# Performance work log

Hardware: AMD Instinct MI355X
Metric: run time of the kernel (lower is better)

Reference implementation:

```python
import jax, jax.numpy as jnp
import numpy as np

EMBED_DIM = 1024
NUM_HEAD = 16
HEAD_DIM = EMBED_DIM // NUM_HEAD


def setup_inputs() -> dict:
    key = jax.random.key(0)
    ks = jax.random.split(key, 9)
    B, S, D = 2, 2048, EMBED_DIM
    scale = 1.0 / np.sqrt(D)
    x = jax.random.normal(ks[0], (B, S, D), dtype=jnp.float32)
    Wq = jax.random.normal(ks[1], (D, D), dtype=jnp.float32) * scale
    bq = jnp.zeros((D,), jnp.float32)
    Wk = jax.random.normal(ks[2], (D, D), dtype=jnp.float32) * scale
    bk = jnp.zeros((D,), jnp.float32)
    Wv = jax.random.normal(ks[3], (D, D), dtype=jnp.float32) * scale
    bv = jnp.zeros((D,), jnp.float32)
    Wfc = jax.random.normal(ks[4], (D, D), dtype=jnp.float32) * scale
    bfc = jnp.zeros((D,), jnp.float32)
    return {"x": x, "Wq": Wq, "bq": bq, "Wk": Wk, "bk": bk,
            "Wv": Wv, "bv": bv, "Wfc": Wfc, "bfc": bfc}


def _split_heads(t):
    B, S, D = t.shape
    return t.reshape(B, S, NUM_HEAD, HEAD_DIM).transpose(0, 2, 1, 3)  # b nh s hd


def reference(x, Wq, bq, Wk, bk, Wv, bv, Wfc, bfc):
    # torch nn.Linear: y = x @ W.T + b
    q = _split_heads(x @ Wq.T + bq)   # [b, nh, s, hd]
    k = _split_heads(x @ Wk.T + bk)   # [b, nh, s, hd]
    v = _split_heads(x @ Wv.T + bv)   # [b, nh, s, hd]
    # Gram matrix K^T K per (batch, head): [b, nh, hd, hd]
    gram = jnp.einsum('bnsh,bnsk->bnhk', k, k)
    gram_inv = jnp.linalg.inv(gram)
    # score = Q (K^T K)^{-1} K^T : [b, nh, s, s]
    q_proj = jnp.einsum('bnsh,bnhk->bnsk', q, gram_inv)
    score = jnp.einsum('bnsk,bntk->bnst', q_proj, k)
    attn = jax.nn.softmax(score / jnp.sqrt(jnp.float32(EMBED_DIM)), axis=-1)
    out = jnp.einsum('bnst,bnth->bnsh', attn, v)  # [b, nh, s, hd]
    B, _, S, _ = out.shape
    out = out.transpose(0, 2, 1, 3).reshape(B, S, EMBED_DIM)
    return out @ Wfc.T + bfc
```

## Files before the change

### kernel.cpp

```cpp
#include <hip/hip_runtime.h>
#include <cstddef>
#include <cstdint>

#define S_LEN 2048
#define NHEAD 16
#define HDIM  64
#define EMB   1024
#define MROWS 4096

typedef short bf16x8 __attribute__((ext_vector_type(8)));
typedef float f32x4 __attribute__((ext_vector_type(4)));

__device__ __forceinline__ unsigned short f2bf(float f) {
  union { float f; unsigned u; } v; v.f = f;
  return (unsigned short)((v.u + 0x8000u) >> 16);
}
__device__ __forceinline__ unsigned pack2bf(float a, float b) {
  union { float f; unsigned u; } x, y; x.f = a; y.f = b;
  return ((x.u + 0x8000u) >> 16) | ((y.u + 0x8000u) & 0xFFFF0000u);
}

__device__ __forceinline__ f32x4 fzero() {
  f32x4 z = {0.0f, 0.0f, 0.0f, 0.0f};
  return z;
}

__global__ __launch_bounds__(256) void cast_kernel(
    const float* __restrict__ x, const float* __restrict__ Wq,
    const float* __restrict__ Wk, const float* __restrict__ Wv,
    const float* __restrict__ Wfc, unsigned short* __restrict__ dst)
{
  size_t idx8 = (size_t)(blockIdx.x * 256 + threadIdx.x) * 8;
  unsigned seg = (unsigned)(idx8 >> 20);
  const float* src;
  size_t off;
  if (seg < 4) { src = x; off = idx8; }
  else {
    const float* w4[4] = {Wq, Wk, Wv, Wfc};
    src = w4[seg - 4];
    off = idx8 & 0xFFFFFu;
  }
  float4 a = *(const float4*)&src[off];
  float4 b = *(const float4*)&src[off + 4];
  uint4 p;
  p.x = pack2bf(a.x, a.y);
  p.y = pack2bf(a.z, a.w);
  p.z = pack2bf(b.x, b.y);
  p.w = pack2bf(b.z, b.w);
  *(uint4*)&dst[idx8] = p;
}

__global__ __launch_bounds__(256) void gemm_qkv(
    const unsigned short* __restrict__ A, const unsigned short* __restrict__ Wall,
    const float* __restrict__ bq, const float* __restrict__ bk,
    const float* __restrict__ bv, unsigned short* __restrict__ Qhd,
    unsigned short* __restrict__ Khd, unsigned short* __restrict__ KTd,
    unsigned short* __restrict__ VTd)
{
  __shared__ short As[128][40];
  __shared__ short Bs[128][40];
  const int z = blockIdx.z;
  const unsigned short* B = Wall + (size_t)z * 1048576;
  const float* bias = (z == 0) ? bq : (z == 1) ? bk : bv;
  unsigned short* Yh = (z == 0) ? Qhd : (z == 1) ? Khd : nullptr;
  unsigned short* Yt = (z == 1) ? KTd : (z == 2) ? VTd : nullptr;
  const int K = EMB;
  const int t = threadIdx.x;
  const int lane = t & 63, w = t >> 6;
  const int quad = lane >> 4, l16 = lane & 15;
  const int wr = w >> 1, wc = w & 1;
  const int m0 = blockIdx.y * 128, n0 = blockIdx.x * 128;
  const int sr = t >> 2, sk = (t & 3) * 8;

  f32x4 acc[4][4];
#pragma unroll
  for (int i = 0; i < 4; ++i)
#pragma unroll
    for (int j = 0; j < 4; ++j) acc[i][j] = fzero();

  float4 pa0 = *(const float4*)&A[(size_t)(m0 + sr) * K + sk];
  float4 pa1 = *(const float4*)&A[(size_t)(m0 + 64 + sr) * K + sk];
  float4 pb0 = *(const float4*)&B[(size_t)(n0 + sr) * K + sk];
  float4 pb1 = *(const float4*)&B[(size_t)(n0 + 64 + sr) * K + sk];

  for (int k0 = 0; k0 < K; k0 += 32) {
    __syncthreads();
    *(float4*)&As[sr][sk] = pa0;
    *(float4*)&As[64 + sr][sk] = pa1;
    *(float4*)&Bs[sr][sk] = pb0;
    *(float4*)&Bs[64 + sr][sk] = pb1;
    __syncthreads();
    if (k0 + 32 < K) {
      pa0 = *(const float4*)&A[(size_t)(m0 + sr) * K + k0 + 32 + sk];
      pa1 = *(const float4*)&A[(size_t)(m0 + 64 + sr) * K + k0 + 32 + sk];
      pb0 = *(const float4*)&B[(size_t)(n0 + sr) * K + k0 + 32 + sk];
      pb1 = *(const float4*)&B[(size_t)(n0 + 64 + sr) * K + k0 + 32 + sk];
    }
    bf16x8 af[4], bfr[4];
#pragma unroll
    for (int i = 0; i < 4; ++i)
      af[i] = *(const bf16x8*)&As[64 * wr + 16 * i + l16][quad * 8];
#pragma unroll
    for (int j = 0; j < 4; ++j)
      bfr[j] = *(const bf16x8*)&Bs[64 * wc + 16 * j + l16][quad * 8];
#pragma unroll
    for (int i = 0; i < 4; ++i)
#pragma unroll
      for (int j = 0; j < 4; ++j)
        acc[i][j] = __builtin_amdgcn_mfma_f32_16x16x32_bf16(af[i], bfr[j], acc[i][j], 0, 0, 0);
  }

#pragma unroll
  for (int i = 0; i < 4; ++i) {
    int mb = m0 + 64 * wr + 16 * i + quad * 4;
#pragma unroll
    for (int j = 0; j < 4; ++j) {
      int n = n0 + 64 * wc + 16 * j + l16;
      float bvv = bias[n];
      int h = n >> 6, d = n & 63;
      if (Yh) {
#pragma unroll
        for (int r = 0; r < 4; ++r) {
          int m = mb + r;
          int b = m >> 11, s = m & 2047;
          Yh[((size_t)(b * NHEAD + h)) * 131072 + (size_t)s * 64 + d] =
              f2bf(acc[i][j][r] + bvv);
        }
      }
      if (Yt) {
        int b = mb >> 11, s = mb & 2047;
        uint2 pk;
        pk.x = pack2bf(acc[i][j][0] + bvv, acc[i][j][1] + bvv);
        pk.y = pack2bf(acc[i][j][2] + bvv, acc[i][j][3] + bvv);
        *(uint2*)&Yt[((size_t)(b * NHEAD + h)) * 131072 + (size_t)d * S_LEN + s] = pk;
      }
    }
  }
}

__global__ __launch_bounds__(256) void gemm_fc(
    const unsigned short* __restrict__ A, const unsigned short* __restrict__ B,
    const float* __restrict__ bias, float* __restrict__ Yf)
{
  __shared__ short As[128][40];
  __shared__ short Bs[128][40];
  const int K = EMB, N = EMB;
  const int t = threadIdx.x;
  const int lane = t & 63, w = t >> 6;
  const int quad = lane >> 4, l16 = lane & 15;
  const int wr = w >> 1, wc = w & 1;
  const int m0 = blockIdx.y * 128, n0 = blockIdx.x * 128;
  const int sr = t >> 2, sk = (t & 3) * 8;

  f32x4 acc[4][4];
#pragma unroll
  for (int i = 0; i < 4; ++i)
#pragma unroll
    for (int j = 0; j < 4; ++j) acc[i][j] = fzero();

  float4 pa0 = *(const float4*)&A[(size_t)(m0 + sr) * K + sk];
  float4 pa1 = *(const float4*)&A[(size_t)(m0 + 64 + sr) * K + sk];
  float4 pb0 = *(const float4*)&B[(size_t)(n0 + sr) * K + sk];
  float4 pb1 = *(const float4*)&B[(size_t)(n0 + 64 + sr) * K + sk];

  for (int k0 = 0; k0 < K; k0 += 32) {
    __syncthreads();
    *(float4*)&As[sr][sk] = pa0;
    *(float4*)&As[64 + sr][sk] = pa1;
    *(float4*)&Bs[sr][sk] = pb0;
    *(float4*)&Bs[64 + sr][sk] = pb1;
    __syncthreads();
    if (k0 + 32 < K) {
      pa0 = *(const float4*)&A[(size_t)(m0 + sr) * K + k0 + 32 + sk];
      pa1 = *(const float4*)&A[(size_t)(m0 + 64 + sr) * K + k0 + 32 + sk];
      pb0 = *(const float4*)&B[(size_t)(n0 + sr) * K + k0 + 32 + sk];
      pb1 = *(const float4*)&B[(size_t)(n0 + 64 + sr) * K + k0 + 32 + sk];
    }
    bf16x8 af[4], bfr[4];
#pragma unroll
    for (int i = 0; i < 4; ++i)
      af[i] = *(const bf16x8*)&As[64 * wr + 16 * i + l16][quad * 8];
#pragma unroll
    for (int j = 0; j < 4; ++j)
      bfr[j] = *(const bf16x8*)&Bs[64 * wc + 16 * j + l16][quad * 8];
#pragma unroll
    for (int i = 0; i < 4; ++i)
#pragma unroll
      for (int j = 0; j < 4; ++j)
        acc[i][j] = __builtin_amdgcn_mfma_f32_16x16x32_bf16(af[i], bfr[j], acc[i][j], 0, 0, 0);
  }

#pragma unroll
  for (int i = 0; i < 4; ++i) {
    int mb = m0 + 64 * wr + 16 * i + quad * 4;
#pragma unroll
    for (int j = 0; j < 4; ++j) {
      int n = n0 + 64 * wc + 16 * j + l16;
      float bvv = bias[n];
#pragma unroll
      for (int r = 0; r < 4; ++r)
        Yf[(size_t)(mb + r) * N + n] = acc[i][j][r] + bvv;
    }
  }
}

__global__ __launch_bounds__(256) void gram_mfma(
    const unsigned short* __restrict__ KTh, float* __restrict__ gram_p)
{
  __shared__ short KTs[64][136];
  const int t = threadIdx.x;
  const int lane = t & 63, w = t >> 6;
  const int quad = lane >> 4, l16 = lane & 15;
  const int bh = blockIdx.x >> 2, part = blockIdx.x & 3;
  const unsigned short* Kb = KTh + (size_t)bh * 131072 + part * 512;

  f32x4 gacc[4];
#pragma unroll
  for (int j = 0; j < 4; ++j) gacc[j] = fzero();

  const int rv = t >> 4, cv = (t & 15) * 8;
  for (int st = 0; st < 4; ++st) {
    float4 vv[4];
#pragma unroll
    for (int r = 0; r < 4; ++r)
      vv[r] = *(const float4*)&Kb[(size_t)(rv + 16 * r) * S_LEN + st * 128 + cv];
    __syncthreads();
#pragma unroll
    for (int r = 0; r < 4; ++r)
      *(float4*)&KTs[rv + 16 * r][cv] = vv[r];
    __syncthreads();
#pragma unroll
    for (int c = 0; c < 4; ++c) {
      bf16x8 ai = *(const bf16x8*)&KTs[16 * w + l16][32 * c + quad * 8];
#pragma unroll
      for (int jb = 0; jb < 4; ++jb) {
        bf16x8 bj = *(const bf16x8*)&KTs[16 * jb + l16][32 * c + quad * 8];
        gacc[jb] = __builtin_amdgcn_mfma_f32_16x16x32_bf16(ai, bj, gacc[jb], 0, 0, 0);
      }
    }
  }
#pragma unroll
  for (int jb = 0; jb < 4; ++jb)
#pragma unroll
    for (int r = 0; r < 4; ++r)
      gram_p[(size_t)blockIdx.x * 4096 +
             (size_t)(16 * w + quad * 4 + r) * 64 + 16 * jb + l16] = gacc[jb][r];
}

__global__ __launch_bounds__(256) void inv_kernel(
    const float* __restrict__ gram_p, unsigned short* __restrict__ ginv)
{
  __shared__ float As[64][68];
  __shared__ float prow[2][64];
  __shared__ float fcol[2][64];
  const int bh = blockIdx.x;
  const int t = threadIdx.x;
  const int r = t >> 2;
  const int c0 = (t & 3) * 16;
  const float* G = gram_p + (size_t)bh * 4 * 4096;

  float4 g[4];
#pragma unroll
  for (int jj = 0; jj < 4; ++jj) {
    int off = r * 64 + c0 + 4 * jj;
    float4 s0 = *(const float4*)&G[off];
    float4 s1 = *(const float4*)&G[4096 + off];
    float4 s2 = *(const float4*)&G[8192 + off];
    float4 s3 = *(const float4*)&G[12288 + off];
    g[jj].x = (s0.x + s1.x) + (s2.x + s3.x);
    g[jj].y = (s0.y + s1.y) + (s2.y + s3.y);
    g[jj].z = (s0.z + s1.z) + (s2.z + s3.z);
    g[jj].w = (s0.w + s1.w) + (s2.w + s3.w);
    *(float4*)&As[r][c0 + 4 * jj] = g[jj];
  }
  if (c0 == 0) fcol[0][r] = g[0].x;
  if (r == 0) {
#pragma unroll
    for (int jj = 0; jj < 4; ++jj) *(float4*)&prow[0][c0 + 4 * jj] = g[jj];
  }
  __syncthreads();

  for (int k = 0; k < 64; ++k) {
    const int kb = k & 1;
    const float f = fcol[kb][r];
    const float ip = 1.0f / fcol[kb][k];
    const float fi = f * ip;
    const bool pr = (r == k);
    float4 nv[4];
#pragma unroll
    for (int jj = 0; jj < 4; ++jj) {
      float4 a = *(const float4*)&As[r][c0 + 4 * jj];
      float4 p = *(const float4*)&prow[kb][c0 + 4 * jj];
      float4 o;
      if (pr) {
        o.x = p.x * ip; o.y = p.y * ip; o.z = p.z * ip; o.w = p.w * ip;
      } else {
        o.x = fmaf(-fi, p.x, a.x); o.y = fmaf(-fi, p.y, a.y);
        o.z = fmaf(-fi, p.z, a.z); o.w = fmaf(-fi, p.w, a.w);
      }
      const int cb = c0 + 4 * jj;
      const float kv = pr ? ip : -fi;
      if (cb == k) o.x = kv;
      if (cb + 1 == k) o.y = kv;
      if (cb + 2 == k) o.z = kv;
      if (cb + 3 == k) o.w = kv;
      *(float4*)&As[r][c0 + 4 * jj] = o;
      nv[jj] = o;
    }
    if (k < 63) {
      const int nk = k + 1, nb = nk & 1;
      if (nk >= c0 && nk < c0 + 16) fcol[nb][r] = As[r][nk];
      if (r == nk) {
#pragma unroll
        for (int jj = 0; jj < 4; ++jj) *(float4*)&prow[nb][c0 + 4 * jj] = nv[jj];
      }
    }
    __syncthreads();
  }

  unsigned short* O = ginv + (size_t)bh * 4096;
#pragma unroll
  for (int jj = 0; jj < 4; ++jj) {
    float4 v = *(const float4*)&As[r][c0 + 4 * jj];
    uint2 pk;
    pk.x = pack2bf(v.x, v.y);
    pk.y = pack2bf(v.z, v.w);
    *(uint2*)&O[r * 64 + c0 + 4 * jj] = pk;
  }
}

__global__ __launch_bounds__(256) void flash_mfma(
    const unsigned short* __restrict__ Qh, const unsigned short* __restrict__ Kh,
    const unsigned short* __restrict__ VTh, const unsigned short* __restrict__ Ginv,
    unsigned short* __restrict__ AO)
{
  __shared__ short Qps[64 * 72];
  __shared__ short Ps[2][64 * 72];
  __shared__ float Lred[4][64];
  const int t = threadIdx.x;
  const int lane = t & 63, w = t >> 6;
  const int quad = lane >> 4, l16 = lane & 15;
  const int qt = blockIdx.x, bh = blockIdx.y;
  const unsigned short* Qb = Qh + (size_t)bh * 131072;
  const unsigned short* Kb = Kh + (size_t)bh * 131072;
  const unsigned short* Vb = VTh + (size_t)bh * 131072;
  const unsigned short* Gb = Ginv + (size_t)bh * 4096;

  {
    bf16x8 aq[2];
#pragma unroll
    for (int c = 0; c < 2; ++c)
      aq[c] = *(const bf16x8*)&Qb[(size_t)(qt * 64 + 16 * w + l16) * 64 + 32 * c + 8 * quad];
    f32x4 qacc[4];
#pragma unroll
    for (int nb = 0; nb < 4; ++nb) qacc[nb] = fzero();
#pragma unroll
    for (int c = 0; c < 2; ++c) {
#pragma unroll
      for (int nb = 0; nb < 4; ++nb) {
        bf16x8 bg = *(const bf16x8*)&Gb[(size_t)(16 * nb + l16) * 64 + 32 * c + 8 * quad];
        qacc[nb] = __builtin_amdgcn_mfma_f32_16x16x32_bf16(aq[c], bg, qacc[nb], 0, 0, 0);
      }
    }
#pragma unroll
    for (int nb = 0; nb < 4; ++nb)
#pragma unroll
      for (int r = 0; r < 4; ++r)
        Qps[(16 * w + 4 * quad + r) * 72 + 16 * nb + l16] =
            (short)f2bf(qacc[nb][r] * 0.03125f);
  }
  __syncthreads();

  f32x4 oacc[4];
#pragma unroll
  for (int qb = 0; qb < 4; ++qb) oacc[qb] = fzero();
  float lsum[4] = {0.0f, 0.0f, 0.0f, 0.0f};

  for (int kt = 0; kt < 32; ++kt) {
    bf16x8 ak[2];
#pragma unroll
    for (int c = 0; c < 2; ++c)
      ak[c] = *(const bf16x8*)&Kb[(size_t)(kt * 64 + 16 * w + l16) * 64 + 32 * c + 8 * quad];
    f32x4 sacc[4];
#pragma unroll
    for (int qb = 0; qb < 4; ++qb) sacc[qb] = fzero();
#pragma unroll
    for (int c = 0; c < 2; ++c) {
#pragma unroll
      for (int qb = 0; qb < 4; ++qb) {
        bf16x8 bq = *(const bf16x8*)&Qps[(16 * qb + l16) * 72 + 32 * c + 8 * quad];
        sacc[qb] = __builtin_amdgcn_mfma_f32_16x16x32_bf16(ak[c], bq, sacc[qb], 0, 0, 0);
      }
    }
    short* Pbuf = &Ps[kt & 1][0];
#pragma unroll
    for (int qb = 0; qb < 4; ++qb) {
      float e0 = __expf(sacc[qb][0]);
      float e1 = __expf(sacc[qb][1]);
      float e2 = __expf(sacc[qb][2]);
      float e3 = __expf(sacc[qb][3]);
      lsum[qb] += (e0 + e1) + (e2 + e3);
      uint2 pk;
      pk.x = pack2bf(e0, e1);
      pk.y = pack2bf(e2, e3);
      *(uint2*)&Pbuf[(16 * qb + l16) * 72 + 16 * w + 4 * quad] = pk;
    }
    __syncthreads();

    bf16x8 av[2];
#pragma unroll
    for (int c = 0; c < 2; ++c)
      av[c] = *(const bf16x8*)&Vb[(size_t)(16 * w + l16) * S_LEN + kt * 64 + 32 * c + 8 * quad];
#pragma unroll
    for (int c = 0; c < 2; ++c) {
#pragma unroll
      for (int qb = 0; qb < 4; ++qb) {
        bf16x8 bp = *(const bf16x8*)&Pbuf[(16 * qb + l16) * 72 + 32 * c + 8 * quad];
        oacc[qb] = __builtin_amdgcn_mfma_f32_16x16x32_bf16(av[c], bp, oacc[qb], 0, 0, 0);
      }
    }
  }

#pragma unroll
  for (int qb = 0; qb < 4; ++qb) {
    lsum[qb] += __shfl_xor(lsum[qb], 16, 64);
    lsum[qb] += __shfl_xor(lsum[qb], 32, 64);
  }
  if (lane < 16)
#pragma unroll
    for (int qb = 0; qb < 4; ++qb) Lred[w][qb * 16 + l16] = lsum[qb];
  __syncthreads();
  if (t < 64)
    Lred[0][t] = 1.0f / (Lred[0][t] + Lred[1][t] + Lred[2][t] + Lred[3][t]);
  __syncthreads();

  const int b = bh >> 4, h = bh & 15;
#pragma unroll
  for (int qb = 0; qb < 4; ++qb) {
    float li = Lred[0][16 * qb + l16];
    int s = qt * 64 + 16 * qb + l16;
    size_t base = (size_t)b * S_LEN * EMB + (size_t)s * EMB + h * 64 + 16 * w + 4 * quad;
#pragma unroll
    for (int r = 0; r < 4; ++r)
      AO[base + r] = f2bf(oacc[qb][r] * li);
  }
}

extern "C" void kernel_launch(void* const* d_in, const int* in_sizes, int n_in,
                              void* d_out, int out_size, void* d_ws, size_t ws_size,
                              hipStream_t stream) {
  (void)in_sizes; (void)n_in; (void)out_size; (void)ws_size;
  const float* x   = (const float*)d_in[0];
  const float* Wq  = (const float*)d_in[1];
  const float* bq  = (const float*)d_in[2];
  const float* Wk  = (const float*)d_in[3];
  const float* bk  = (const float*)d_in[4];
  const float* Wv  = (const float*)d_in[5];
  const float* bv  = (const float*)d_in[6];
  const float* Wfc = (const float*)d_in[7];
  const float* bfc = (const float*)d_in[8];
  float* out = (float*)d_out;

  unsigned short* xb   = (unsigned short*)d_ws;
  unsigned short* Wqb  = xb + (size_t)4194304;
  unsigned short* Wfcb = Wqb + 3 * 1048576;
  unsigned short* Qhd  = Wfcb + 1048576;
  unsigned short* Khd  = Qhd + 4194304;
  unsigned short* KTd  = Khd + 4194304;
  unsigned short* VTd  = KTd + 4194304;
  unsigned short* AOd  = VTd + 4194304;
  float* gram_p        = (float*)(AOd + 4194304);
  unsigned short* ginv = (unsigned short*)(gram_p + 524288);

  cast_kernel<<<4096, 256, 0, stream>>>(x, Wq, Wk, Wv, Wfc, xb);
  gemm_qkv<<<dim3(8, 32, 3), 256, 0, stream>>>(xb, Wqb, bq, bk, bv,
                                               Qhd, Khd, KTd, VTd);
  gram_mfma<<<128, 256, 0, stream>>>(KTd, gram_p);
  inv_kernel<<<32, 256, 0, stream>>>(gram_p, ginv);
  flash_mfma<<<dim3(S_LEN / 64, 32), 256, 0, stream>>>(Qhd, Khd, VTd, ginv, AOd);
  gemm_fc<<<dim3(8, 32), 256, 0, stream>>>(AOd, Wfcb, bfc, out);
}
```

Measured before the change: 285.9 us.

## Drop K transpose buffer, stage V transpose via LDS, tune flash and fc kernels

Removes the separate transposed-K output from the QKV GEMM, so the gram kernel reads row-major K and transposes it in shared memory. V^T is now written through an LDS staging tile with 16-byte coalesced stores. The flash kernel keeps Q fragments in registers, prefetches the next K tile, swaps exp for exp2 with a log2e-folded scale, remaps blocks for L2 locality, sets an occupancy hint and stages its output through LDS for vectorized stores. The fc GEMM uses a 64-wide N tile to double the block count. These changes target global memory traffic, uncoalesced writes and load latency, at the cost of more shared memory and some LDS bank conflicts in the gram transpose.

Result: faster. 280.1 us (-2.0%).

```diff
diff --git a/kernel.cpp b/kernel.cpp
--- a/kernel.cpp
+++ b/kernel.cpp
@@ -54,16 +54,14 @@
     const unsigned short* __restrict__ A, const unsigned short* __restrict__ Wall,
     const float* __restrict__ bq, const float* __restrict__ bk,
     const float* __restrict__ bv, unsigned short* __restrict__ Qhd,
-    unsigned short* __restrict__ Khd, unsigned short* __restrict__ KTd,
-    unsigned short* __restrict__ VTd)
+    unsigned short* __restrict__ Khd, unsigned short* __restrict__ VTd)
 {
   __shared__ short As[128][40];
   __shared__ short Bs[128][40];
+  __shared__ short Ts[64][136];
   const int z = blockIdx.z;
   const unsigned short* B = Wall + (size_t)z * 1048576;
   const float* bias = (z == 0) ? bq : (z == 1) ? bk : bv;
-  unsigned short* Yh = (z == 0) ? Qhd : (z == 1) ? Khd : nullptr;
-  unsigned short* Yt = (z == 1) ? KTd : (z == 2) ? VTd : nullptr;
   const int K = EMB;
   const int t = threadIdx.x;
   const int lane = t & 63, w = t >> 6;
@@ -110,15 +108,16 @@
         acc[i][j] = __builtin_amdgcn_mfma_f32_16x16x32_bf16(af[i], bfr[j], acc[i][j], 0, 0, 0);
   }
 
-#pragma unroll
-  for (int i = 0; i < 4; ++i) {
-    int mb = m0 + 64 * wr + 16 * i + quad * 4;
-#pragma unroll
-    for (int j = 0; j < 4; ++j) {
-      int n = n0 + 64 * wc + 16 * j + l16;
-      float bvv = bias[n];
-      int h = n >> 6, d = n & 63;
-      if (Yh) {
+  if (z < 2) {
+    unsigned short* Yh = (z == 0) ? Qhd : Khd;
+#pragma unroll
+    for (int i = 0; i < 4; ++i) {
+      int mb = m0 + 64 * wr + 16 * i + quad * 4;
+#pragma unroll
+      for (int j = 0; j < 4; ++j) {
+        int n = n0 + 64 * wc + 16 * j + l16;
+        float bvv = bias[n];
+        int h = n >> 6, d = n & 63;
 #pragma unroll
         for (int r = 0; r < 4; ++r) {
           int m = mb + r;
@@ -127,13 +126,35 @@
               f2bf(acc[i][j][r] + bvv);
         }
       }
-      if (Yt) {
-        int b = mb >> 11, s = mb & 2047;
-        uint2 pk;
-        pk.x = pack2bf(acc[i][j][0] + bvv, acc[i][j][1] + bvv);
-        pk.y = pack2bf(acc[i][j][2] + bvv, acc[i][j][3] + bvv);
-        *(uint2*)&Yt[((size_t)(b * NHEAD + h)) * 131072 + (size_t)d * S_LEN + s] = pk;
-      }
+    }
+  } else {
+#pragma unroll
+    for (int hh = 0; hh < 2; ++hh) {
+      __syncthreads();
+      if (wc == hh) {
+#pragma unroll
+        for (int i = 0; i < 4; ++i)
+#pragma unroll
+          for (int j = 0; j < 4; ++j) {
+            int n = n0 + 64 * wc + 16 * j + l16;
+            float bvv = bias[n];
+            int dl = 16 * j + l16;
+            uint2 pk;
+            pk.x = pack2bf(acc[i][j][0] + bvv, acc[i][j][1] + bvv);
+            pk.y = pack2bf(acc[i][j][2] + bvv, acc[i][j][3] + bvv);
+            *(uint2*)&Ts[dl][64 * wr + 16 * i + 4 * quad] = pk;
+          }
+      }
+      __syncthreads();
+      int dl = t >> 2, s0 = (t & 3) * 32;
+      int n = n0 + 64 * hh + dl;
+      int h = n >> 6, d = n & 63;
+      int b = m0 >> 11, sbase = (m0 & 2047) + s0;
+      unsigned short* dst =
+          &VTd[((size_t)(b * NHEAD + h)) * 131072 + (size_t)d * S_LEN + sbase];
+#pragma unroll
+      for (int k2 = 0; k2 < 4; ++k2)
+        *(uint4*)&dst[8 * k2] = *(const uint4*)&Ts[dl][s0 + 8 * k2];
     }
   }
 }
@@ -143,50 +164,47 @@
     const float* __restrict__ bias, float* __restrict__ Yf)
 {
   __shared__ short As[128][40];
-  __shared__ short Bs[128][40];
+  __shared__ short Bs[64][40];
   const int K = EMB, N = EMB;
   const int t = threadIdx.x;
   const int lane = t & 63, w = t >> 6;
   const int quad = lane >> 4, l16 = lane & 15;
   const int wr = w >> 1, wc = w & 1;
-  const int m0 = blockIdx.y * 128, n0 = blockIdx.x * 128;
+  const int m0 = blockIdx.y * 128, n0 = blockIdx.x * 64;
   const int sr = t >> 2, sk = (t & 3) * 8;
 
-  f32x4 acc[4][4];
+  f32x4 acc[4][2];
 #pragma unroll
   for (int i = 0; i < 4; ++i)
 #pragma unroll
-    for (int j = 0; j < 4; ++j) acc[i][j] = fzero();
+    for (int j = 0; j < 2; ++j) acc[i][j] = fzero();
 
   float4 pa0 = *(const float4*)&A[(size_t)(m0 + sr) * K + sk];
   float4 pa1 = *(const float4*)&A[(size_t)(m0 + 64 + sr) * K + sk];
   float4 pb0 = *(const float4*)&B[(size_t)(n0 + sr) * K + sk];
-  float4 pb1 = *(const float4*)&B[(size_t)(n0 + 64 + sr) * K + sk];
 
   for (int k0 = 0; k0 < K; k0 += 32) {
     __syncthreads();
     *(float4*)&As[sr][sk] = pa0;
     *(float4*)&As[64 + sr][sk] = pa1;
-    *(float4*)&Bs[sr][sk] = pb0;
-    *(float4*)&Bs[64 + sr][sk] = pb1;
+    if (sr < 64) *(float4*)&Bs[sr][sk] = pb0;
     __syncthreads();
     if (k0 + 32 < K) {
       pa0 = *(const float4*)&A[(size_t)(m0 + sr) * K + k0 + 32 + sk];
       pa1 = *(const float4*)&A[(size_t)(m0 + 64 + sr) * K + k0 + 32 + sk];
       pb0 = *(const float4*)&B[(size_t)(n0 + sr) * K + k0 + 32 + sk];
-      pb1 = *(const float4*)&B[(size_t)(n0 + 64 + sr) * K + k0 + 32 + sk];
-    }
-    bf16x8 af[4], bfr[4];
+    }
+    bf16x8 af[4], bfr[2];
 #pragma unroll
     for (int i = 0; i < 4; ++i)
       af[i] = *(const bf16x8*)&As[64 * wr + 16 * i + l16][quad * 8];
 #pragma unroll
-    for (int j = 0; j < 4; ++j)
-      bfr[j] = *(const bf16x8*)&Bs[64 * wc + 16 * j + l16][quad * 8];
+    for (int j = 0; j < 2; ++j)
+      bfr[j] = *(const bf16x8*)&Bs[32 * wc + 16 * j + l16][quad * 8];
 #pragma unroll
     for (int i = 0; i < 4; ++i)
 #pragma unroll
-      for (int j = 0; j < 4; ++j)
+      for (int j = 0; j < 2; ++j)
         acc[i][j] = __builtin_amdgcn_mfma_f32_16x16x32_bf16(af[i], bfr[j], acc[i][j], 0, 0, 0);
   }
 
@@ -194,8 +212,8 @@
   for (int i = 0; i < 4; ++i) {
     int mb = m0 + 64 * wr + 16 * i + quad * 4;
 #pragma unroll
-    for (int j = 0; j < 4; ++j) {
-      int n = n0 + 64 * wc + 16 * j + l16;
+    for (int j = 0; j < 2; ++j) {
+      int n = n0 + 32 * wc + 16 * j + l16;
       float bvv = bias[n];
 #pragma unroll
       for (int r = 0; r < 4; ++r)
@@ -205,29 +223,35 @@
 }
 
 __global__ __launch_bounds__(256) void gram_mfma(
-    const unsigned short* __restrict__ KTh, float* __restrict__ gram_p)
+    const unsigned short* __restrict__ Khd, float* __restrict__ gram_p)
 {
   __shared__ short KTs[64][136];
   const int t = threadIdx.x;
   const int lane = t & 63, w = t >> 6;
   const int quad = lane >> 4, l16 = lane & 15;
   const int bh = blockIdx.x >> 2, part = blockIdx.x & 3;
-  const unsigned short* Kb = KTh + (size_t)bh * 131072 + part * 512;
+  const unsigned short* Kb = Khd + (size_t)bh * 131072 + (size_t)part * 512 * 64;
 
   f32x4 gacc[4];
 #pragma unroll
   for (int j = 0; j < 4; ++j) gacc[j] = fzero();
 
-  const int rv = t >> 4, cv = (t & 15) * 8;
+  const int r8 = t >> 1;
+  const int c8 = (t & 1) * 32;
   for (int st = 0; st < 4; ++st) {
-    float4 vv[4];
-#pragma unroll
-    for (int r = 0; r < 4; ++r)
-      vv[r] = *(const float4*)&Kb[(size_t)(rv + 16 * r) * S_LEN + st * 128 + cv];
-    __syncthreads();
-#pragma unroll
-    for (int r = 0; r < 4; ++r)
-      *(float4*)&KTs[rv + 16 * r][cv] = vv[r];
+    float4 kv[4];
+#pragma unroll
+    for (int i = 0; i < 4; ++i)
+      kv[i] = *(const float4*)&Kb[(size_t)(st * 128 + r8) * 64 + c8 + 8 * i];
+    __syncthreads();
+#pragma unroll
+    for (int i = 0; i < 4; ++i) {
+      union { float4 f; unsigned short h[8]; } u;
+      u.f = kv[i];
+#pragma unroll
+      for (int jj = 0; jj < 8; ++jj)
+        KTs[c8 + 8 * i + jj][r8] = (short)u.h[jj];
+    }
     __syncthreads();
 #pragma unroll
     for (int c = 0; c < 4; ++c) {
@@ -329,7 +353,7 @@
   }
 }
 
-__global__ __launch_bounds__(256) void flash_mfma(
+__global__ __launch_bounds__(256, 4) void flash_mfma(
     const unsigned short* __restrict__ Qh, const unsigned short* __restrict__ Kh,
     const unsigned short* __restrict__ VTh, const unsigned short* __restrict__ Ginv,
     unsigned short* __restrict__ AO)
@@ -340,12 +364,18 @@
   const int t = threadIdx.x;
   const int lane = t & 63, w = t >> 6;
   const int quad = lane >> 4, l16 = lane & 15;
-  const int qt = blockIdx.x, bh = blockIdx.y;
+  const int id = blockIdx.x;
+  const int qt = (id >> 3) & 31;
+  const int bh = ((id >> 8) << 3) | (id & 7);
   const unsigned short* Qb = Qh + (size_t)bh * 131072;
   const unsigned short* Kb = Kh + (size_t)bh * 131072;
   const unsigned short* Vb = VTh + (size_t)bh * 131072;
   const unsigned short* Gb = Ginv + (size_t)bh * 4096;
 
+  bf16x8 ak[2];
+#pragma unroll
+  for (int c = 0; c < 2; ++c)
+    ak[c] = *(const bf16x8*)&Kb[(size_t)(16 * w + l16) * 64 + 32 * c + 8 * quad];
   {
     bf16x8 aq[2];
 #pragma unroll
@@ -362,14 +392,22 @@
         qacc[nb] = __builtin_amdgcn_mfma_f32_16x16x32_bf16(aq[c], bg, qacc[nb], 0, 0, 0);
       }
     }
+    const float cs = 0.04508422f;
 #pragma unroll
     for (int nb = 0; nb < 4; ++nb)
 #pragma unroll
       for (int r = 0; r < 4; ++r)
         Qps[(16 * w + 4 * quad + r) * 72 + 16 * nb + l16] =
-            (short)f2bf(qacc[nb][r] * 0.03125f);
+            (short)f2bf(qacc[nb][r] * cs);
   }
   __syncthreads();
+
+  bf16x8 bqf[2][4];
+#pragma unroll
+  for (int c = 0; c < 2; ++c)
+#pragma unroll
+    for (int qb = 0; qb < 4; ++qb)
+      bqf[c][qb] = *(const bf16x8*)&Qps[(16 * qb + l16) * 72 + 32 * c + 8 * quad];
 
   f32x4 oacc[4];
 #pragma unroll
@@ -377,28 +415,32 @@
   float lsum[4] = {0.0f, 0.0f, 0.0f, 0.0f};
 
   for (int kt = 0; kt < 32; ++kt) {
-    bf16x8 ak[2];
+    bf16x8 av[2];
 #pragma unroll
     for (int c = 0; c < 2; ++c)
-      ak[c] = *(const bf16x8*)&Kb[(size_t)(kt * 64 + 16 * w + l16) * 64 + 32 * c + 8 * quad];
+      av[c] = *(const bf16x8*)&Vb[(size_t)(16 * w + l16) * S_LEN + kt * 64 + 32 * c + 8 * quad];
+
     f32x4 sacc[4];
 #pragma unroll
     for (int qb = 0; qb < 4; ++qb) sacc[qb] = fzero();
 #pragma unroll
-    for (int c = 0; c < 2; ++c) {
-#pragma unroll
-      for (int qb = 0; qb < 4; ++qb) {
-        bf16x8 bq = *(const bf16x8*)&Qps[(16 * qb + l16) * 72 + 32 * c + 8 * quad];
-        sacc[qb] = __builtin_amdgcn_mfma_f32_16x16x32_bf16(ak[c], bq, sacc[qb], 0, 0, 0);
-      }
-    }
+    for (int c = 0; c < 2; ++c)
+#pragma unroll
+      for (int qb = 0; qb < 4; ++qb)
+        sacc[qb] = __builtin_amdgcn_mfma_f32_16x16x32_bf16(ak[c], bqf[c][qb], sacc[qb], 0, 0, 0);
+
+    const int nk = (kt + 1) & 31;
+#pragma unroll
+    for (int c = 0; c < 2; ++c)
+      ak[c] = *(const bf16x8*)&Kb[(size_t)(nk * 64 + 16 * w + l16) * 64 + 32 * c + 8 * quad];
+
     short* Pbuf = &Ps[kt & 1][0];
 #pragma unroll
     for (int qb = 0; qb < 4; ++qb) {
-      float e0 = __expf(sacc[qb][0]);
-      float e1 = __expf(sacc[qb][1]);
-      float e2 = __expf(sacc[qb][2]);
-      float e3 = __expf(sacc[qb][3]);
+      float e0 = exp2f(sacc[qb][0]);
+      float e1 = exp2f(sacc[qb][1]);
+      float e2 = exp2f(sacc[qb][2]);
+      float e3 = exp2f(sacc[qb][3]);
       lsum[qb] += (e0 + e1) + (e2 + e3);
       uint2 pk;
       pk.x = pack2bf(e0, e1);
@@ -407,18 +449,13 @@
     }
     __syncthreads();
 
-    bf16x8 av[2];
 #pragma unroll
     for (int c = 0; c < 2; ++c)
-      av[c] = *(const bf16x8*)&Vb[(size_t)(16 * w + l16) * S_LEN + kt * 64 + 32 * c + 8 * quad];
-#pragma unroll
-    for (int c = 0; c < 2; ++c) {
 #pragma unroll
       for (int qb = 0; qb < 4; ++qb) {
         bf16x8 bp = *(const bf16x8*)&Pbuf[(16 * qb + l16) * 72 + 32 * c + 8 * quad];
         oacc[qb] = __builtin_amdgcn_mfma_f32_16x16x32_bf16(av[c], bp, oacc[qb], 0, 0, 0);
       }
-    }
   }
 
 #pragma unroll
@@ -434,15 +471,23 @@
     Lred[0][t] = 1.0f / (Lred[0][t] + Lred[1][t] + Lred[2][t] + Lred[3][t]);
   __syncthreads();
 
-  const int b = bh >> 4, h = bh & 15;
 #pragma unroll
   for (int qb = 0; qb < 4; ++qb) {
     float li = Lred[0][16 * qb + l16];
-    int s = qt * 64 + 16 * qb + l16;
-    size_t base = (size_t)b * S_LEN * EMB + (size_t)s * EMB + h * 64 + 16 * w + 4 * quad;
-#pragma unroll
-    for (int r = 0; r < 4; ++r)
-      AO[base + r] = f2bf(oacc[qb][r] * li);
+    uint2 pk;
+    pk.x = pack2bf(oacc[qb][0] * li, oacc[qb][1] * li);
+    pk.y = pack2bf(oacc[qb][2] * li, oacc[qb][3] * li);
+    *(uint2*)&Qps[(16 * qb + l16) * 72 + 16 * w + 4 * quad] = pk;
+  }
+  __syncthreads();
+  {
+    const int b = bh >> 4, h = bh & 15;
+    int q = t >> 2, d0 = (t & 3) * 16;
+    uint4 v0 = *(const uint4*)&Qps[q * 72 + d0];
+    uint4 v1 = *(const uint4*)&Qps[q * 72 + d0 + 8];
+    size_t base = (size_t)b * S_LEN * EMB + (size_t)(qt * 64 + q) * EMB + h * 64 + d0;
+    *(uint4*)&AO[base] = v0;
+    *(uint4*)&AO[base + 8] = v1;
   }
 }
 
@@ -466,17 +511,16 @@
   unsigned short* Wfcb = Wqb + 3 * 1048576;
   unsigned short* Qhd  = Wfcb + 1048576;
   unsigned short* Khd  = Qhd + 4194304;
-  unsigned short* KTd  = Khd + 4194304;
-  unsigned short* VTd  = KTd + 4194304;
+  unsigned short* VTd  = Khd + 4194304;
   unsigned short* AOd  = VTd + 4194304;
   float* gram_p        = (float*)(AOd + 4194304);
   unsigned short* ginv = (unsigned short*)(gram_p + 524288);
 
   cast_kernel<<<4096, 256, 0, stream>>>(x, Wq, Wk, Wv, Wfc, xb);
   gemm_qkv<<<dim3(8, 32, 3), 256, 0, stream>>>(xb, Wqb, bq, bk, bv,
-                                               Qhd, Khd, KTd, VTd);
-  gram_mfma<<<128, 256, 0, stream>>>(KTd, gram_p);
+                                               Qhd, Khd, VTd);
+  gram_mfma<<<128, 256, 0, stream>>>(Khd, gram_p);
   inv_kernel<<<32, 256, 0, stream>>>(gram_p, ginv);
-  flash_mfma<<<dim3(S_LEN / 64, 32), 256, 0, stream>>>(Qhd, Khd, VTd, ginv, AOd);
-  gemm_fc<<<dim3(8, 32), 256, 0, stream>>>(AOd, Wfcb, bfc, out);
-}
+  flash_mfma<<<1024, 256, 0, stream>>>(Qhd, Khd, VTd, ginv, AOd);
+  gemm_fc<<<dim3(16, 32), 256, 0, stream>>>(AOd, Wfcb, bfc, out);
+}
```
